# Kernel tuning notes

Measured on AMD Instinct MI355X. Metric: run time of the kernel, lower is better.

Reference implementation:

```python
import jax, jax.numpy as jnp
import numpy as np
from jax import lax

DIM = 128
HEADS = 4
HEAD_DIM = DIM // HEADS          # 32
SR = 2
BN_EPS = 1e-5


def setup_inputs() -> dict:
    key = jax.random.key(0)
    ks = jax.random.split(key, 16)
    B, N, C = 8, 3136, DIM
    H = W = 56
    Nkv = (H // SR) * (W // SR)  # 784
    s = 0.05
    inp = {
        "x": jax.random.normal(ks[0], (B, N, C), jnp.float32),
        "relative_pos": jax.random.normal(ks[1], (HEADS, N, Nkv), jnp.float32),
        "Wq": jax.random.normal(ks[2], (C, C), jnp.float32) * s,
        "bq": jnp.zeros((C,), jnp.float32),
        "Wk": jax.random.normal(ks[3], (C, C), jnp.float32) * s,
        "bk": jnp.zeros((C,), jnp.float32),
        "Wv": jax.random.normal(ks[4], (C, C), jnp.float32) * s,
        "bv": jnp.zeros((C,), jnp.float32),
        "conv_w": jax.random.normal(ks[5], (C, 1, SR, SR), jnp.float32) * s,  # depthwise OIHW
        "conv_b": jnp.zeros((C,), jnp.float32),
        "bn_gamma": jnp.ones((C,), jnp.float32),
        "bn_beta": jnp.zeros((C,), jnp.float32),
        "bn_mean": jax.random.normal(ks[6], (C,), jnp.float32) * 0.1,
        "bn_var": jax.random.uniform(ks[7], (C,), jnp.float32, 0.5, 1.5),
        "Wp": jax.random.normal(ks[8], (C, C), jnp.float32) * s,
        "bp": jnp.zeros((C,), jnp.float32),
        "H": H,
        "W": W,
    }
    return inp


def reference(x, relative_pos, Wq, bq, Wk, bk, Wv, bv, conv_w, conv_b,
              bn_gamma, bn_beta, bn_mean, bn_var, Wp, bp, H, W):
    B, N, C = x.shape
    scale = HEAD_DIM ** -0.5

    # q: (B, heads, N, head_dim)
    q = (x @ Wq + bq).reshape(B, N, HEADS, HEAD_DIM).transpose(0, 2, 1, 3)

    # spatial reduction: depthwise conv stride SR + BatchNorm (eval, running stats)
    x_img = x.transpose(0, 2, 1).reshape(B, C, H, W)
    y = lax.conv_general_dilated(
        x_img, conv_w, window_strides=(SR, SR), padding="VALID",
        feature_group_count=C,
        dimension_numbers=("NCHW", "OIHW", "NCHW")) + conv_b[None, :, None, None]
    inv = bn_gamma * lax.rsqrt(bn_var + BN_EPS)
    y = y * inv[None, :, None, None] + (bn_beta - bn_mean * inv)[None, :, None, None]
    x_ = y.reshape(B, C, -1).transpose(0, 2, 1)  # (B, Nkv, C)
    Nkv = x_.shape[1]

    k = (x_ @ Wk + bk).reshape(B, Nkv, HEADS, HEAD_DIM).transpose(0, 2, 1, 3)
    v = (x_ @ Wv + bv).reshape(B, Nkv, HEADS, HEAD_DIM).transpose(0, 2, 1, 3)

    attn = jnp.einsum("bhnd,bhmd->bhnm", q, k) * scale + relative_pos[None]
    attn = jax.nn.softmax(attn, axis=-1)
    out = jnp.einsum("bhnm,bhmd->bhnd", attn, v)
    out = out.transpose(0, 2, 1, 3).reshape(B, N, C)
    return out @ Wp + bp
```

## Files before the change

kernel.cpp:

```cpp
#include <hip/hip_runtime.h>
#include <hip/hip_bf16.h>

#define BATCH 8
#define NQ 3136
#define CDIM 128
#define NHEAD 4
#define HD 32
#define NKV 784
#define HIMG 56
#define SCALE 0.17677669529663687f

typedef __attribute__((ext_vector_type(8))) short bf8_t;
typedef __attribute__((ext_vector_type(4))) float f4_t;

using bf16 = __hip_bfloat16;
using u16  = unsigned short;

static __device__ __forceinline__ float b2f(bf16 v){ return __bfloat162float(v); }
static __device__ __forceinline__ bf16  f2b(float v){ return __float2bfloat16(v); }
static __device__ __forceinline__ short f2s(float v){
  union { bf16 b; short s; } u; u.b = f2b(v); return u.s;
}
static __device__ __forceinline__ float u16f(u16 x){
  union { u16 u; bf16 b; } c; c.u = x; return b2f(c.b);
}
static __device__ __forceinline__ float ld1(const void* p, size_t i, int f){
  return f ? b2f(((const bf16*)p)[i]) : ((const float*)p)[i];
}
static __device__ __forceinline__ bf8_t ld8(const void* p, size_t i, int f){
  if (f) return *(const bf8_t*)((const bf16*)p + i);
  const float* fp = (const float*)p + i;
  float4 a = *(const float4*)fp;
  float4 b = *(const float4*)(fp + 4);
  bf8_t r;
  r[0]=f2s(a.x); r[1]=f2s(a.y); r[2]=f2s(a.z); r[3]=f2s(a.w);
  r[4]=f2s(b.x); r[5]=f2s(b.y); r[6]=f2s(b.z); r[7]=f2s(b.w);
  return r;
}
static __device__ __forceinline__ int detect_flag(const void* var_raw){
  const u16* h = (const u16*)var_raw;
  int lane = threadIdx.x & 63;
  bool ok = true;
  #pragma unroll
  for (int t = 0; t < 2; t++){
    union { u16 u; bf16 b; } cv; cv.u = h[lane + 64*t];
    float v = b2f(cv.b);
    ok = ok && (v > 0.3f) && (v < 1.7f);
  }
  return (__ballot(ok) == ~0ull) ? 1 : 0;
}

static __device__ __forceinline__ void mfma_row(
    const bf8_t a[4], const bf16* __restrict__ Wt, int m, int g, f4_t acc[8])
{
  #pragma unroll
  for (int ct = 0; ct < 8; ct++){
    f4_t c = {0.f,0.f,0.f,0.f};
    const bf16* bp = Wt + (size_t)(ct*16 + m)*CDIM + 8*g;
    #pragma unroll
    for (int ks = 0; ks < 4; ks++){
      bf8_t b = *(const bf8_t*)(bp + 32*ks);
      c = __builtin_amdgcn_mfma_f32_16x16x32_bf16(a[ks], b, c, 0,0,0);
    }
    acc[ct] = c;
  }
}

__global__ __launch_bounds__(256) void prep_kernel(
    const void* __restrict__ Wq, const void* __restrict__ Wk,
    const void* __restrict__ Wv, const void* __restrict__ Wp,
    const void* __restrict__ var, const void* __restrict__ cw,
    const void* __restrict__ cb, const void* __restrict__ gam,
    const void* __restrict__ bet, const void* __restrict__ mea,
    const void* __restrict__ bq, const void* __restrict__ bk,
    const void* __restrict__ bv, const void* __restrict__ bp,
    bf16* __restrict__ Wqt, bf16* __restrict__ Wkt,
    bf16* __restrict__ Wvt, bf16* __restrict__ Wpt,
    bf16* __restrict__ bqs, bf16* __restrict__ bks,
    bf16* __restrict__ bvs, bf16* __restrict__ bps,
    float* __restrict__ cwf, float* __restrict__ inv, float* __restrict__ shift2)
{
  int f = detect_flag(var);
  int idx = blockIdx.x*256 + threadIdx.x;
  int mat = idx >> 14;
  int e   = idx & 16383;
  int o = e >> 7, i = e & 127;
  const void* src; bf16* dst; float s = 1.f;
  if      (mat == 0){ src = Wq; dst = Wqt; s = SCALE; }
  else if (mat == 1){ src = Wk; dst = Wkt; }
  else if (mat == 2){ src = Wv; dst = Wvt; }
  else              { src = Wp; dst = Wpt; }
  dst[e] = f2b(ld1(src, (size_t)i*128 + o, f) * s);

  if (blockIdx.x == 0){
    int t = threadIdx.x;
    cwf[t]       = ld1(cw, t, f);
    cwf[t + 256] = ld1(cw, t + 256, f);
    if (t < 128){
      bqs[t] = f2b(ld1(bq, t, f) * SCALE);
      bks[t] = f2b(ld1(bk, t, f));
      bvs[t] = f2b(ld1(bv, t, f));
      bps[t] = f2b(ld1(bp, t, f));
      float iv = ld1(gam, t, f) * rsqrtf(ld1(var, t, f) + 1e-5f);
      inv[t] = iv;
      shift2[t] = ld1(bet, t, f) - ld1(mea, t, f) * iv + ld1(cb, t, f) * iv;
    }
  }
}

__global__ __launch_bounds__(256) void fat_kernel(
    const void* __restrict__ x, const void* __restrict__ var,
    const float* __restrict__ cwf, const float* __restrict__ inv,
    const float* __restrict__ shift2, bf16* __restrict__ xr,
    const bf16* __restrict__ Wqt, const bf16* __restrict__ bqs,
    bf16* __restrict__ qbf,
    const void* __restrict__ rel, bf16* __restrict__ relb, int qblk)
{
  int f = detect_flag(var);
  if (blockIdx.x < 3136){
    int idx = blockIdx.x*256 + threadIdx.x;
    int c  = idx & 127;
    int t  = idx >> 7;
    int b  = t / NKV;
    int kv = t - b*NKV;
    int i = kv/28, j = kv - i*28;
    size_t base = (size_t)(b*NQ + 2*i*HIMG + 2*j)*CDIM + c;
    float acc = ld1(x, base, f)                   * cwf[c*4 + 0]
              + ld1(x, base + CDIM, f)            * cwf[c*4 + 1]
              + ld1(x, base + HIMG*CDIM, f)       * cwf[c*4 + 2]
              + ld1(x, base + HIMG*CDIM + CDIM, f)* cwf[c*4 + 3];
    xr[idx] = f2b(acc * inv[c] + shift2[c]);
  } else if ((int)blockIdx.x < 3136 + qblk){
    int wave = threadIdx.x >> 6, lane = threadIdx.x & 63;
    int m = lane & 15, g = lane >> 4;
    int task = (blockIdx.x - 3136)*4 + wave;
    int row0 = task*16;
    bf8_t a[4];
    #pragma unroll
    for (int ks = 0; ks < 4; ks++)
      a[ks] = ld8(x, (size_t)(row0 + m)*CDIM + 8*g + 32*ks, f);
    f4_t acc[8];
    mfma_row(a, Wqt, m, g, acc);
    #pragma unroll
    for (int ct = 0; ct < 8; ct++){
      int col = ct*16 + m;
      float bv = b2f(bqs[col]);
      #pragma unroll
      for (int r = 0; r < 4; r++)
        qbf[(size_t)(row0 + 4*g + r)*CDIM + col] = f2b(acc[ct][r] + bv);
    }
  } else {
    if (f) return;
    int bi = blockIdx.x - 3136 - qblk;
    size_t gid = ((size_t)bi*256 + threadIdx.x)*8;
    const float* fp = (const float*)rel + gid;
    float4 a  = *(const float4*)fp;
    float4 b4 = *(const float4*)(fp + 4);
    union { u16 hh[8]; uint4 u4; } pk;
    pk.hh[0]=(u16)f2s(a.x);  pk.hh[1]=(u16)f2s(a.y);
    pk.hh[2]=(u16)f2s(a.z);  pk.hh[3]=(u16)f2s(a.w);
    pk.hh[4]=(u16)f2s(b4.x); pk.hh[5]=(u16)f2s(b4.y);
    pk.hh[6]=(u16)f2s(b4.z); pk.hh[7]=(u16)f2s(b4.w);
    *(uint4*)(relb + gid) = pk.u4;
  }
}

__global__ __launch_bounds__(256) void kv_kernel(
    const bf16* __restrict__ xr,
    const bf16* __restrict__ Wkt, const bf16* __restrict__ Wvt,
    const bf16* __restrict__ bks, const bf16* __restrict__ bvs,
    bf16* __restrict__ kbf, bf16* __restrict__ vtb)
{
  int wave = threadIdx.x >> 6, lane = threadIdx.x & 63;
  int m = lane & 15, g = lane >> 4;
  bool isK = blockIdx.x < 98;
  int bx = isK ? blockIdx.x : blockIdx.x - 98;
  int row0 = (bx*4 + wave)*16;
  bf8_t a[4];
  #pragma unroll
  for (int ks = 0; ks < 4; ks++)
    a[ks] = *(const bf8_t*)(xr + (size_t)(row0 + m)*CDIM + 8*g + 32*ks);
  f4_t acc[8];
  mfma_row(a, isK ? Wkt : Wvt, m, g, acc);

  if (isK){
    #pragma unroll
    for (int ct = 0; ct < 8; ct++){
      int col = ct*16 + m;
      float bv = b2f(bks[col]);
      #pragma unroll
      for (int r = 0; r < 4; r++)
        kbf[(size_t)(row0 + 4*g + r)*CDIM + col] = f2b(acc[ct][r] + bv);
    }
  } else {
    int b   = row0 / NKV;
    int kv0 = row0 - b*NKV + 4*g;
    #pragma unroll
    for (int ct = 0; ct < 8; ct++){
      int col = ct*16 + m;
      float bv = b2f(bvs[col]);
      int h = col >> 5, d = col & 31;
      union { bf16 hh[4]; uint2 u; } pk;
      #pragma unroll
      for (int r = 0; r < 4; r++) pk.hh[r] = f2b(acc[ct][r] + bv);
      *(uint2*)(vtb + (size_t)((b*NHEAD + h)*HD + d)*NKV + kv0) = pk.u;
    }
  }
}

template<int RM> struct RelT { using T = float4; };
template<> struct RelT<1> { using T = uint2; };

template<int RM>
static __device__ __forceinline__ typename RelT<RM>::T relld(const void* relp, int off){
  if constexpr (RM == 1) return *(const uint2*)((const bf16*)relp + off);
  else                   return *(const float4*)((const float*)relp + off);
}
template<int RM>
static __device__ __forceinline__ float relget(const typename RelT<RM>::T& v, int r){
  if constexpr (RM == 1){
    union { uint2 u; u16 h[4]; } c; c.u = v;
    return u16f(c.h[r]);
  } else {
    return r == 0 ? v.x : (r == 1 ? v.y : (r == 2 ? v.z : v.w));
  }
}

template<int RM>
static __device__ __forceinline__ void attn_run(
    const void* __restrict__ relp, const bf16* __restrict__ kbase,
    const bf16* __restrict__ vb0, const bf16* __restrict__ vb1,
    bf16* __restrict__ pl, int m, int g,
    bf8_t q8, float& m_run, float& l_run, f4_t& O0, f4_t& O1)
{
  using RT = typename RelT<RM>::T;
  RT rl[8], rt;
  #pragma unroll
  for (int t = 0; t < 8; t++) rl[t] = relld<RM>(relp, 16*t + 4*g);

  #pragma unroll 1
  for (int c = 0; c < 6; c++){
    int kv0 = c*128;
    f4_t s[8];
    #pragma unroll
    for (int t = 0; t < 8; t++){
      bf8_t k8 = *(const bf8_t*)(kbase + (size_t)(kv0 + t*16)*CDIM);
      f4_t z = {0.f,0.f,0.f,0.f};
      s[t] = __builtin_amdgcn_mfma_f32_16x16x32_bf16(k8, q8, z, 0,0,0);
    }
    #pragma unroll
    for (int t = 0; t < 8; t++)
      #pragma unroll
      for (int r = 0; r < 4; r++)
        s[t][r] += relget<RM>(rl[t], r);
    if (c < 5){
      #pragma unroll
      for (int t = 0; t < 8; t++)
        rl[t] = relld<RM>(relp, kv0 + 128 + 16*t + 4*g);
    } else {
      rt = relld<RM>(relp, 768 + 4*g);
    }
    float vmax = s[0][0];
    #pragma unroll
    for (int t = 0; t < 8; t++)
      #pragma unroll
      for (int r = 0; r < 4; r++)
        if (t + r > 0) vmax = fmaxf(vmax, s[t][r]);
    vmax = fmaxf(vmax, __shfl_xor(vmax, 16, 64));
    vmax = fmaxf(vmax, __shfl_xor(vmax, 32, 64));
    float mn = fmaxf(m_run, vmax);
    float al = __expf(m_run - mn);
    m_run = mn;
    l_run *= al;
    float alT[4];
    #pragma unroll
    for (int r = 0; r < 4; r++) alT[r] = __shfl(al, 4*g + r, 64);
    #pragma unroll
    for (int r = 0; r < 4; r++){ O0[r] *= alT[r]; O1[r] *= alT[r]; }
    float lsum = 0.f;
    #pragma unroll
    for (int t = 0; t < 8; t++){
      union { u16 h[4]; uint2 u; } pk;
      #pragma unroll
      for (int r = 0; r < 4; r++){
        float p = __expf(s[t][r] - m_run);
        lsum += p;
        pk.h[r] = (u16)f2s(p);
      }
      *(uint2*)(pl + m*136 + 16*t + 4*g) = pk.u;
    }
    l_run += lsum;
    #pragma unroll
    for (int ks = 0; ks < 4; ks++){
      bf8_t a8 = *(const bf8_t*)(pl + m*136 + ks*32 + 8*g);
      bf8_t v0 = *(const bf8_t*)(vb0 + kv0 + ks*32 + 8*g);
      bf8_t v1 = *(const bf8_t*)(vb1 + kv0 + ks*32 + 8*g);
      O0 = __builtin_amdgcn_mfma_f32_16x16x32_bf16(a8, v0, O0, 0,0,0);
      O1 = __builtin_amdgcn_mfma_f32_16x16x32_bf16(a8, v1, O1, 0,0,0);
    }
  }
  {
    bf8_t k8 = *(const bf8_t*)(kbase + (size_t)768*CDIM);
    f4_t z = {0.f,0.f,0.f,0.f};
    f4_t s1 = __builtin_amdgcn_mfma_f32_16x16x32_bf16(k8, q8, z, 0,0,0);
    #pragma unroll
    for (int r = 0; r < 4; r++) s1[r] += relget<RM>(rt, r);
    float vmax = s1[0];
    #pragma unroll
    for (int r = 1; r < 4; r++) vmax = fmaxf(vmax, s1[r]);
    vmax = fmaxf(vmax, __shfl_xor(vmax, 16, 64));
    vmax = fmaxf(vmax, __shfl_xor(vmax, 32, 64));
    float mn = fmaxf(m_run, vmax);
    float al = __expf(m_run - mn);
    m_run = mn;
    l_run *= al;
    float alT[4];
    #pragma unroll
    for (int r = 0; r < 4; r++) alT[r] = __shfl(al, 4*g + r, 64);
    #pragma unroll
    for (int r = 0; r < 4; r++){ O0[r] *= alT[r]; O1[r] *= alT[r]; }
    float lsum = 0.f;
    union { u16 h[4]; uint2 u; } pk;
    #pragma unroll
    for (int r = 0; r < 4; r++){
      float p = __expf(s1[r] - m_run);
      lsum += p;
      pk.h[r] = (u16)f2s(p);
    }
    *(uint2*)(pl + m*136 + 4*g) = pk.u;
    l_run += lsum;
    bf8_t a8, v0, v1;
    if (g >= 2){
      bf8_t z8 = {0,0,0,0,0,0,0,0};
      a8 = z8; v0 = z8; v1 = z8;
    } else {
      a8 = *(const bf8_t*)(pl + m*136 + 8*g);
      v0 = *(const bf8_t*)(vb0 + 768 + 8*g);
      v1 = *(const bf8_t*)(vb1 + 768 + 8*g);
    }
    O0 = __builtin_amdgcn_mfma_f32_16x16x32_bf16(a8, v0, O0, 0,0,0);
    O1 = __builtin_amdgcn_mfma_f32_16x16x32_bf16(a8, v1, O1, 0,0,0);
  }
}

template<int QF>
__global__ __launch_bounds__(256) void attn_kernel(
    const bf16* __restrict__ qbf, const void* __restrict__ x,
    const bf16* __restrict__ Wqt, const bf16* __restrict__ bqs,
    const bf16* __restrict__ kb, const bf16* __restrict__ vtb,
    const void* __restrict__ rel, const bf16* __restrict__ relb,
    const void* __restrict__ var,
    void* __restrict__ dout, bf16* __restrict__ obf)
{
  int f = detect_flag(var);
  int wave = threadIdx.x >> 6, lane = threadIdx.x & 63;
  int m = lane & 15, g = lane >> 4;
  int qt = blockIdx.x, h = blockIdx.y, b = blockIdx.z;
  int qrow0 = qt*64 + wave*16;

  __shared__ bf16 Plds[4][16*136];
  bf16* pl = Plds[wave];

  bf8_t q8;
  if constexpr (QF == 0){
    q8 = *(const bf8_t*)(qbf + (size_t)(b*NQ + qrow0 + m)*CDIM + h*HD + 8*g);
  } else {
    bf8_t xa[4];
    #pragma unroll
    for (int ks = 0; ks < 4; ks++)
      xa[ks] = ld8(x, (size_t)(b*NQ + qrow0 + m)*CDIM + 8*g + 32*ks, f);
    f4_t qc0 = {0.f,0.f,0.f,0.f}, qc1 = {0.f,0.f,0.f,0.f};
    const bf16* wp0 = Wqt + (size_t)(h*HD + m)*CDIM + 8*g;
    const bf16* wp1 = Wqt + (size_t)(h*HD + 16 + m)*CDIM + 8*g;
    #pragma unroll
    for (int ks = 0; ks < 4; ks++){
      bf8_t w0 = *(const bf8_t*)(wp0 + 32*ks);
      bf8_t w1 = *(const bf8_t*)(wp1 + 32*ks);
      qc0 = __builtin_amdgcn_mfma_f32_16x16x32_bf16(xa[ks], w0, qc0, 0,0,0);
      qc1 = __builtin_amdgcn_mfma_f32_16x16x32_bf16(xa[ks], w1, qc1, 0,0,0);
    }
    float bv0 = b2f(bqs[h*HD + m]);
    float bv1 = b2f(bqs[h*HD + 16 + m]);
    #pragma unroll
    for (int r = 0; r < 4; r++){
      pl[(4*g + r)*136 + m]      = f2b(qc0[r] + bv0);
      pl[(4*g + r)*136 + 16 + m] = f2b(qc1[r] + bv1);
    }
    q8 = *(const bf8_t*)(pl + m*136 + 8*g);
  }

  const bf16* kbase = kb  + (size_t)(b*NKV + m)*CDIM + h*HD + 8*g;
  const bf16* vb0   = vtb + (size_t)((b*NHEAD + h)*HD + m)*NKV;
  const bf16* vb1   = vtb + (size_t)((b*NHEAD + h)*HD + 16 + m)*NKV;
  size_t rrow = ((size_t)h*NQ + qrow0 + m)*(size_t)NKV;

  float m_run = -1e30f, l_run = 0.f;
  f4_t O0 = {0.f,0.f,0.f,0.f}, O1 = {0.f,0.f,0.f,0.f};

  if (f){
    attn_run<1>((const void*)((const bf16*)rel + rrow), kbase, vb0, vb1,
                pl, m, g, q8, m_run, l_run, O0, O1);
  } else if (relb != nullptr){
    attn_run<1>((const void*)(relb + rrow), kbase, vb0, vb1,
                pl, m, g, q8, m_run, l_run, O0, O1);
  } else {
    attn_run<0>((const void*)((const float*)rel + rrow), kbase, vb0, vb1,
                pl, m, g, q8, m_run, l_run, O0, O1);
  }

  l_run += __shfl_xor(l_run, 16, 64);
  l_run += __shfl_xor(l_run, 32, 64);
  float lT[4];
  #pragma unroll
  for (int r = 0; r < 4; r++) lT[r] = __shfl(l_run, 4*g + r, 64);

  bf16* ob = f ? (bf16*)dout : obf;
  size_t orow = (size_t)(b*NQ + qrow0 + 4*g);
  #pragma unroll
  for (int r = 0; r < 4; r++){
    float iv = 1.0f / lT[r];
    ob[(orow + r)*CDIM + h*HD + m]      = f2b(O0[r] * iv);
    ob[(orow + r)*CDIM + h*HD + 16 + m] = f2b(O1[r] * iv);
  }
}

__global__ __launch_bounds__(256) void proj_kernel(
    const bf16* A0, const bf16* A1, const bf16* __restrict__ Wt,
    const bf16* __restrict__ bias, void* outp, const void* __restrict__ var)
{
  int f = detect_flag(var);
  const bf16* A = f ? A0 : A1;
  int wave = threadIdx.x >> 6, lane = threadIdx.x & 63;
  int m = lane & 15, g = lane >> 4;
  int row0 = (blockIdx.x*4 + wave)*16;
  bf8_t a[4];
  #pragma unroll
  for (int ks = 0; ks < 4; ks++)
    a[ks] = *(const bf8_t*)(A + (size_t)(row0 + m)*CDIM + 8*g + 32*ks);
  f4_t acc[8];
  mfma_row(a, Wt, m, g, acc);
  #pragma unroll
  for (int ct = 0; ct < 8; ct++){
    int col = ct*16 + m;
    float bv = b2f(bias[col]);
    #pragma unroll
    for (int r = 0; r < 4; r++){
      size_t oi = (size_t)(row0 + 4*g + r)*CDIM + col;
      float v = acc[ct][r] + bv;
      if (f) ((bf16*)outp)[oi]  = f2b(v);
      else   ((float*)outp)[oi] = v;
    }
  }
}

extern "C" void kernel_launch(void* const* d_in, const int* in_sizes, int n_in,
                              void* d_out, int out_size, void* d_ws, size_t ws_size,
                              hipStream_t stream)
{
  const void* x   = d_in[0];
  const void* rel = d_in[1];
  const void* Wq  = d_in[2];
  const void* bq  = d_in[3];
  const void* Wk  = d_in[4];
  const void* bk  = d_in[5];
  const void* Wv  = d_in[6];
  const void* bv  = d_in[7];
  const void* cw  = d_in[8];
  const void* cb  = d_in[9];
  const void* gam = d_in[10];
  const void* bet = d_in[11];
  const void* mea = d_in[12];
  const void* var = d_in[13];
  const void* Wp  = d_in[14];
  const void* bp  = d_in[15];

  char* w = (char*)d_ws;
  auto alloc = [&](size_t bytes){
    char* p = w; w += (bytes + 255) & ~(size_t)255; return p;
  };
  bf16* Wqt = (bf16*)alloc(128*128*sizeof(bf16));
  bf16* Wkt = (bf16*)alloc(128*128*sizeof(bf16));
  bf16* Wvt = (bf16*)alloc(128*128*sizeof(bf16));
  bf16* Wpt = (bf16*)alloc(128*128*sizeof(bf16));
  bf16* bqs = (bf16*)alloc(128*sizeof(bf16));
  bf16* bks = (bf16*)alloc(128*sizeof(bf16));
  bf16* bvs = (bf16*)alloc(128*sizeof(bf16));
  bf16* bps = (bf16*)alloc(128*sizeof(bf16));
  float* cwf    = (float*)alloc(512*sizeof(float));
  float* inv    = (float*)alloc(128*sizeof(float));
  float* shift2 = (float*)alloc(128*sizeof(float));
  bf16* xr  = (bf16*)alloc((size_t)BATCH*NKV*CDIM*sizeof(bf16));
  bf16* kbf = (bf16*)alloc((size_t)BATCH*NKV*CDIM*sizeof(bf16));
  bf16* vtb = (bf16*)alloc((size_t)BATCH*NKV*CDIM*sizeof(bf16));
  bf16* obf = (bf16*)alloc((size_t)BATCH*NQ*CDIM*sizeof(bf16));

  size_t relb_bytes = (size_t)NHEAD*NQ*NKV*sizeof(bf16);
  bf16* relb = nullptr;
  if (((char*)d_ws + ws_size) - w >= (ptrdiff_t)(relb_bytes + 256))
    relb = (bf16*)alloc(relb_bytes);

  size_t qbf_bytes = (size_t)BATCH*NQ*CDIM*sizeof(bf16);
  bool use_q = (((char*)d_ws + ws_size) - w) >= (ptrdiff_t)(qbf_bytes + 256);
  bf16* qbf = use_q ? (bf16*)alloc(qbf_bytes) : nullptr;

  int qblk = use_q ? 392 : 0;
  int rblk = relb  ? 4802 : 0;

  prep_kernel<<<256, 256, 0, stream>>>(Wq, Wk, Wv, Wp, var, cw, cb, gam, bet, mea,
                                       bq, bk, bv, bp,
                                       Wqt, Wkt, Wvt, Wpt, bqs, bks, bvs, bps,
                                       cwf, inv, shift2);
  fat_kernel<<<3136 + qblk + rblk, 256, 0, stream>>>(
      x, var, cwf, inv, shift2, xr, Wqt, bqs, qbf, rel, relb, qblk);
  kv_kernel<<<196, 256, 0, stream>>>(xr, Wkt, Wvt, bks, bvs, kbf, vtb);
  dim3 ag(49, NHEAD, BATCH);
  if (use_q)
    attn_kernel<0><<<ag, 256, 0, stream>>>(
        qbf, x, Wqt, bqs, kbf, vtb, rel, relb, var, d_out, obf);
  else
    attn_kernel<1><<<ag, 256, 0, stream>>>(
        qbf, x, Wqt, bqs, kbf, vtb, rel, relb, var, d_out, obf);
  proj_kernel<<<392, 256, 0, stream>>>((const bf16*)d_out, obf, Wpt, bps, d_out, var);
}
```

Measured before the change: 230.5 us.

## Split attention KV chunks to 64, transpose PV MFMA, vectorize conv reduction

The attention inner loop now processes 64-key chunks instead of 128, with double-buffered relative-position prefetch, and a launch-bounds hint asks for more waves per SIMD. Swapping the MFMA operand order for P·V puts the output row-wise per lane. That removes the cross-lane shuffles for the rescale factor and the final normalisation, and lets the output be written as packed 4-element stores. The depthwise conv/BN stage processes 4 channels per thread with float4 loads and a transposed weight layout, cutting its block count by four. The catch is more online-softmax rescale steps per row, and register pressure under the tighter launch bound may cause spills.

```diff
diff --git a/kernel.cpp b/kernel.cpp
--- a/kernel.cpp
+++ b/kernel.cpp
@@ -26,6 +26,13 @@
 }
 static __device__ __forceinline__ float ld1(const void* p, size_t i, int f){
   return f ? b2f(((const bf16*)p)[i]) : ((const float*)p)[i];
+}
+static __device__ __forceinline__ float4 ld4f(const void* p, size_t i, int f){
+  if (f){
+    ushort4 u = *(const ushort4*)((const bf16*)p + i);
+    return make_float4(u16f(u.x), u16f(u.y), u16f(u.z), u16f(u.w));
+  }
+  return *(const float4*)((const float*)p + i);
 }
 static __device__ __forceinline__ bf8_t ld8(const void* p, size_t i, int f){
   if (f) return *(const bf8_t*)((const bf16*)p + i);
@@ -94,8 +101,8 @@
 
   if (blockIdx.x == 0){
     int t = threadIdx.x;
-    cwf[t]       = ld1(cw, t, f);
-    cwf[t + 256] = ld1(cw, t + 256, f);
+    { int e2 = t;       cwf[(e2&3)*128 + (e2>>2)] = ld1(cw, e2, f); }
+    { int e2 = t + 256; cwf[(e2&3)*128 + (e2>>2)] = ld1(cw, e2, f); }
     if (t < 128){
       bqs[t] = f2b(ld1(bq, t, f) * SCALE);
       bks[t] = f2b(ld1(bk, t, f));
@@ -117,23 +124,35 @@
     const void* __restrict__ rel, bf16* __restrict__ relb, int qblk)
 {
   int f = detect_flag(var);
-  if (blockIdx.x < 3136){
+  if (blockIdx.x < 784){
     int idx = blockIdx.x*256 + threadIdx.x;
-    int c  = idx & 127;
-    int t  = idx >> 7;
+    int c0 = (idx & 31)*4;
+    int t  = idx >> 5;
     int b  = t / NKV;
     int kv = t - b*NKV;
     int i = kv/28, j = kv - i*28;
-    size_t base = (size_t)(b*NQ + 2*i*HIMG + 2*j)*CDIM + c;
-    float acc = ld1(x, base, f)                   * cwf[c*4 + 0]
-              + ld1(x, base + CDIM, f)            * cwf[c*4 + 1]
-              + ld1(x, base + HIMG*CDIM, f)       * cwf[c*4 + 2]
-              + ld1(x, base + HIMG*CDIM + CDIM, f)* cwf[c*4 + 3];
-    xr[idx] = f2b(acc * inv[c] + shift2[c]);
-  } else if ((int)blockIdx.x < 3136 + qblk){
+    size_t base = (size_t)(b*NQ + 2*i*HIMG + 2*j)*CDIM + c0;
+    float4 t0 = ld4f(x, base, f);
+    float4 t1 = ld4f(x, base + CDIM, f);
+    float4 t2 = ld4f(x, base + HIMG*CDIM, f);
+    float4 t3 = ld4f(x, base + HIMG*CDIM + CDIM, f);
+    float4 w0 = *(const float4*)(cwf + c0);
+    float4 w1 = *(const float4*)(cwf + 128 + c0);
+    float4 w2 = *(const float4*)(cwf + 256 + c0);
+    float4 w3 = *(const float4*)(cwf + 384 + c0);
+    float4 iv4 = *(const float4*)(inv + c0);
+    float4 sh4 = *(const float4*)(shift2 + c0);
+    union { u16 h[4]; uint2 u; } pk;
+    float a;
+    a = t0.x*w0.x + t1.x*w1.x + t2.x*w2.x + t3.x*w3.x; pk.h[0] = (u16)f2s(a*iv4.x + sh4.x);
+    a = t0.y*w0.y + t1.y*w1.y + t2.y*w2.y + t3.y*w3.y; pk.h[1] = (u16)f2s(a*iv4.y + sh4.y);
+    a = t0.z*w0.z + t1.z*w1.z + t2.z*w2.z + t3.z*w3.z; pk.h[2] = (u16)f2s(a*iv4.z + sh4.z);
+    a = t0.w*w0.w + t1.w*w1.w + t2.w*w2.w + t3.w*w3.w; pk.h[3] = (u16)f2s(a*iv4.w + sh4.w);
+    *(uint2*)(xr + (size_t)t*CDIM + c0) = pk.u;
+  } else if ((int)blockIdx.x < 784 + qblk){
     int wave = threadIdx.x >> 6, lane = threadIdx.x & 63;
     int m = lane & 15, g = lane >> 4;
-    int task = (blockIdx.x - 3136)*4 + wave;
+    int task = (blockIdx.x - 784)*4 + wave;
     int row0 = task*16;
     bf8_t a[4];
     #pragma unroll
@@ -151,7 +170,7 @@
     }
   } else {
     if (f) return;
-    int bi = blockIdx.x - 3136 - qblk;
+    int bi = blockIdx.x - 784 - qblk;
     size_t gid = ((size_t)bi*256 + threadIdx.x)*8;
     const float* fp = (const float*)rel + gid;
     float4 a  = *(const float4*)fp;
@@ -208,21 +227,83 @@
   }
 }
 
-template<int RM> struct RelT { using T = float4; };
-template<> struct RelT<1> { using T = uint2; };
+template<int RM> struct RelV { using T = float4; };
+template<> struct RelV<1> { using T = uint2; };
 
 template<int RM>
-static __device__ __forceinline__ typename RelT<RM>::T relld(const void* relp, int off){
+static __device__ __forceinline__ typename RelV<RM>::T relld(const void* relp, int off){
   if constexpr (RM == 1) return *(const uint2*)((const bf16*)relp + off);
   else                   return *(const float4*)((const float*)relp + off);
 }
 template<int RM>
-static __device__ __forceinline__ float relget(const typename RelT<RM>::T& v, int r){
+static __device__ __forceinline__ float relget(const typename RelV<RM>::T& v, int r){
   if constexpr (RM == 1){
     union { uint2 u; u16 h[4]; } c; c.u = v;
     return u16f(c.h[r]);
   } else {
     return r == 0 ? v.x : (r == 1 ? v.y : (r == 2 ? v.z : v.w));
+  }
+}
+template<int RM>
+static __device__ __forceinline__ void ldrel4(
+    typename RelV<RM>::T rl[4], const void* relp, int off){
+  #pragma unroll
+  for (int t = 0; t < 4; t++) rl[t] = relld<RM>(relp, off + 16*t);
+}
+
+template<int RM>
+static __device__ __forceinline__ void chunk64(
+    int kv0, const typename RelV<RM>::T rl[4],
+    const bf16* __restrict__ kbase, const bf16* __restrict__ vb0,
+    const bf16* __restrict__ vb1, bf16* __restrict__ pl, int m, int g,
+    bf8_t q8, float& m_run, float& l_run, f4_t& O0, f4_t& O1)
+{
+  f4_t s[4];
+  #pragma unroll
+  for (int t = 0; t < 4; t++){
+    bf8_t k8 = *(const bf8_t*)(kbase + (size_t)(kv0 + t*16)*CDIM);
+    f4_t z = {0.f,0.f,0.f,0.f};
+    s[t] = __builtin_amdgcn_mfma_f32_16x16x32_bf16(k8, q8, z, 0,0,0);
+  }
+  #pragma unroll
+  for (int t = 0; t < 4; t++)
+    #pragma unroll
+    for (int r = 0; r < 4; r++)
+      s[t][r] += relget<RM>(rl[t], r);
+  float vmax = s[0][0];
+  #pragma unroll
+  for (int t = 0; t < 4; t++)
+    #pragma unroll
+    for (int r = 0; r < 4; r++)
+      if (t + r > 0) vmax = fmaxf(vmax, s[t][r]);
+  vmax = fmaxf(vmax, __shfl_xor(vmax, 16, 64));
+  vmax = fmaxf(vmax, __shfl_xor(vmax, 32, 64));
+  float mn = fmaxf(m_run, vmax);
+  float al = __expf(m_run - mn);
+  m_run = mn;
+  l_run *= al;
+  #pragma unroll
+  for (int r = 0; r < 4; r++){ O0[r] *= al; O1[r] *= al; }
+  float lsum = 0.f;
+  #pragma unroll
+  for (int t = 0; t < 4; t++){
+    union { u16 h[4]; uint2 u; } pk;
+    #pragma unroll
+    for (int r = 0; r < 4; r++){
+      float p = __expf(s[t][r] - m_run);
+      lsum += p;
+      pk.h[r] = (u16)f2s(p);
+    }
+    *(uint2*)(pl + m*136 + t*16 + 4*g) = pk.u;
+  }
+  l_run += lsum;
+  #pragma unroll
+  for (int ks = 0; ks < 2; ks++){
+    bf8_t a8 = *(const bf8_t*)(pl + m*136 + ks*32 + 8*g);
+    bf8_t v0 = *(const bf8_t*)(vb0 + kv0 + ks*32 + 8*g);
+    bf8_t v1 = *(const bf8_t*)(vb1 + kv0 + ks*32 + 8*g);
+    O0 = __builtin_amdgcn_mfma_f32_16x16x32_bf16(v0, a8, O0, 0,0,0);
+    O1 = __builtin_amdgcn_mfma_f32_16x16x32_bf16(v1, a8, O1, 0,0,0);
   }
 }
 
@@ -233,94 +314,35 @@
     bf16* __restrict__ pl, int m, int g,
     bf8_t q8, float& m_run, float& l_run, f4_t& O0, f4_t& O1)
 {
-  using RT = typename RelT<RM>::T;
-  RT rl[8], rt;
-  #pragma unroll
-  for (int t = 0; t < 8; t++) rl[t] = relld<RM>(relp, 16*t + 4*g);
-
+  using RT = typename RelV<RM>::T;
+  RT rlA[4], rlB[4], rtv;
+  ldrel4<RM>(rlA, relp, 4*g);
   #pragma unroll 1
-  for (int c = 0; c < 6; c++){
-    int kv0 = c*128;
-    f4_t s[8];
-    #pragma unroll
-    for (int t = 0; t < 8; t++){
-      bf8_t k8 = *(const bf8_t*)(kbase + (size_t)(kv0 + t*16)*CDIM);
-      f4_t z = {0.f,0.f,0.f,0.f};
-      s[t] = __builtin_amdgcn_mfma_f32_16x16x32_bf16(k8, q8, z, 0,0,0);
-    }
-    #pragma unroll
-    for (int t = 0; t < 8; t++)
-      #pragma unroll
-      for (int r = 0; r < 4; r++)
-        s[t][r] += relget<RM>(rl[t], r);
-    if (c < 5){
-      #pragma unroll
-      for (int t = 0; t < 8; t++)
-        rl[t] = relld<RM>(relp, kv0 + 128 + 16*t + 4*g);
-    } else {
-      rt = relld<RM>(relp, 768 + 4*g);
-    }
-    float vmax = s[0][0];
-    #pragma unroll
-    for (int t = 0; t < 8; t++)
-      #pragma unroll
-      for (int r = 0; r < 4; r++)
-        if (t + r > 0) vmax = fmaxf(vmax, s[t][r]);
+  for (int c2 = 0; c2 < 6; c2++){
+    int kv0 = c2*128;
+    ldrel4<RM>(rlB, relp, kv0 + 64 + 4*g);
+    chunk64<RM>(kv0, rlA, kbase, vb0, vb1, pl, m, g, q8, m_run, l_run, O0, O1);
+    if (c2 < 5) ldrel4<RM>(rlA, relp, kv0 + 128 + 4*g);
+    else        rtv = relld<RM>(relp, 768 + 4*g);
+    chunk64<RM>(kv0 + 64, rlB, kbase, vb0, vb1, pl, m, g, q8, m_run, l_run, O0, O1);
+  }
+  {
+    bf8_t k8 = *(const bf8_t*)(kbase + (size_t)768*CDIM);
+    f4_t z = {0.f,0.f,0.f,0.f};
+    f4_t s1 = __builtin_amdgcn_mfma_f32_16x16x32_bf16(k8, q8, z, 0,0,0);
+    #pragma unroll
+    for (int r = 0; r < 4; r++) s1[r] += relget<RM>(rtv, r);
+    float vmax = fmaxf(fmaxf(s1[0], s1[1]), fmaxf(s1[2], s1[3]));
     vmax = fmaxf(vmax, __shfl_xor(vmax, 16, 64));
     vmax = fmaxf(vmax, __shfl_xor(vmax, 32, 64));
     float mn = fmaxf(m_run, vmax);
     float al = __expf(m_run - mn);
     m_run = mn;
     l_run *= al;
-    float alT[4];
-    #pragma unroll
-    for (int r = 0; r < 4; r++) alT[r] = __shfl(al, 4*g + r, 64);
-    #pragma unroll
-    for (int r = 0; r < 4; r++){ O0[r] *= alT[r]; O1[r] *= alT[r]; }
+    #pragma unroll
+    for (int r = 0; r < 4; r++){ O0[r] *= al; O1[r] *= al; }
+    union { u16 h[4]; uint2 u; } pk;
     float lsum = 0.f;
-    #pragma unroll
-    for (int t = 0; t < 8; t++){
-      union { u16 h[4]; uint2 u; } pk;
-      #pragma unroll
-      for (int r = 0; r < 4; r++){
-        float p = __expf(s[t][r] - m_run);
-        lsum += p;
-        pk.h[r] = (u16)f2s(p);
-      }
-      *(uint2*)(pl + m*136 + 16*t + 4*g) = pk.u;
-    }
-    l_run += lsum;
-    #pragma unroll
-    for (int ks = 0; ks < 4; ks++){
-      bf8_t a8 = *(const bf8_t*)(pl + m*136 + ks*32 + 8*g);
-      bf8_t v0 = *(const bf8_t*)(vb0 + kv0 + ks*32 + 8*g);
-      bf8_t v1 = *(const bf8_t*)(vb1 + kv0 + ks*32 + 8*g);
-      O0 = __builtin_amdgcn_mfma_f32_16x16x32_bf16(a8, v0, O0, 0,0,0);
-      O1 = __builtin_amdgcn_mfma_f32_16x16x32_bf16(a8, v1, O1, 0,0,0);
-    }
-  }
-  {
-    bf8_t k8 = *(const bf8_t*)(kbase + (size_t)768*CDIM);
-    f4_t z = {0.f,0.f,0.f,0.f};
-    f4_t s1 = __builtin_amdgcn_mfma_f32_16x16x32_bf16(k8, q8, z, 0,0,0);
-    #pragma unroll
-    for (int r = 0; r < 4; r++) s1[r] += relget<RM>(rt, r);
-    float vmax = s1[0];
-    #pragma unroll
-    for (int r = 1; r < 4; r++) vmax = fmaxf(vmax, s1[r]);
-    vmax = fmaxf(vmax, __shfl_xor(vmax, 16, 64));
-    vmax = fmaxf(vmax, __shfl_xor(vmax, 32, 64));
-    float mn = fmaxf(m_run, vmax);
-    float al = __expf(m_run - mn);
-    m_run = mn;
-    l_run *= al;
-    float alT[4];
-    #pragma unroll
-    for (int r = 0; r < 4; r++) alT[r] = __shfl(al, 4*g + r, 64);
-    #pragma unroll
-    for (int r = 0; r < 4; r++){ O0[r] *= alT[r]; O1[r] *= alT[r]; }
-    float lsum = 0.f;
-    union { u16 h[4]; uint2 u; } pk;
     #pragma unroll
     for (int r = 0; r < 4; r++){
       float p = __expf(s1[r] - m_run);
@@ -338,13 +360,13 @@
       v0 = *(const bf8_t*)(vb0 + 768 + 8*g);
       v1 = *(const bf8_t*)(vb1 + 768 + 8*g);
     }
-    O0 = __builtin_amdgcn_mfma_f32_16x16x32_bf16(a8, v0, O0, 0,0,0);
-    O1 = __builtin_amdgcn_mfma_f32_16x16x32_bf16(a8, v1, O1, 0,0,0);
-  }
-}
-
-template<int QF>
-__global__ __launch_bounds__(256) void attn_kernel(
+    O0 = __builtin_amdgcn_mfma_f32_16x16x32_bf16(v0, a8, O0, 0,0,0);
+    O1 = __builtin_amdgcn_mfma_f32_16x16x32_bf16(v1, a8, O1, 0,0,0);
+  }
+}
+
+template<int QF, int FB>
+static __device__ __forceinline__ void attn_device(
     const bf16* __restrict__ qbf, const void* __restrict__ x,
     const bf16* __restrict__ Wqt, const bf16* __restrict__ bqs,
     const bf16* __restrict__ kb, const bf16* __restrict__ vtb,
@@ -397,31 +419,54 @@
   float m_run = -1e30f, l_run = 0.f;
   f4_t O0 = {0.f,0.f,0.f,0.f}, O1 = {0.f,0.f,0.f,0.f};
 
-  if (f){
-    attn_run<1>((const void*)((const bf16*)rel + rrow), kbase, vb0, vb1,
-                pl, m, g, q8, m_run, l_run, O0, O1);
-  } else if (relb != nullptr){
-    attn_run<1>((const void*)(relb + rrow), kbase, vb0, vb1,
-                pl, m, g, q8, m_run, l_run, O0, O1);
+  if constexpr (FB == 0){
+    const void* rsrc = f ? (const void*)((const bf16*)rel + rrow)
+                         : (const void*)(relb + rrow);
+    attn_run<1>(rsrc, kbase, vb0, vb1, pl, m, g, q8, m_run, l_run, O0, O1);
   } else {
-    attn_run<0>((const void*)((const float*)rel + rrow), kbase, vb0, vb1,
-                pl, m, g, q8, m_run, l_run, O0, O1);
+    if (f) attn_run<1>((const void*)((const bf16*)rel + rrow), kbase, vb0, vb1,
+                       pl, m, g, q8, m_run, l_run, O0, O1);
+    else   attn_run<0>((const void*)((const float*)rel + rrow), kbase, vb0, vb1,
+                       pl, m, g, q8, m_run, l_run, O0, O1);
   }
 
   l_run += __shfl_xor(l_run, 16, 64);
   l_run += __shfl_xor(l_run, 32, 64);
-  float lT[4];
-  #pragma unroll
-  for (int r = 0; r < 4; r++) lT[r] = __shfl(l_run, 4*g + r, 64);
-
-  bf16* ob = f ? (bf16*)dout : obf;
-  size_t orow = (size_t)(b*NQ + qrow0 + 4*g);
+  float iv = 1.0f / l_run;
+
+  bf16* ob = (f ? (bf16*)dout : obf)
+           + (size_t)(b*NQ + qrow0 + m)*CDIM + h*HD;
+  union { u16 h4[4]; uint2 u; } o0, o1;
   #pragma unroll
   for (int r = 0; r < 4; r++){
-    float iv = 1.0f / lT[r];
-    ob[(orow + r)*CDIM + h*HD + m]      = f2b(O0[r] * iv);
-    ob[(orow + r)*CDIM + h*HD + 16 + m] = f2b(O1[r] * iv);
-  }
+    o0.h4[r] = (u16)f2s(O0[r] * iv);
+    o1.h4[r] = (u16)f2s(O1[r] * iv);
+  }
+  *(uint2*)(ob + 4*g)      = o0.u;
+  *(uint2*)(ob + 16 + 4*g) = o1.u;
+}
+
+template<int QF>
+__global__ __launch_bounds__(256, 6) void attn_kernel(
+    const bf16* __restrict__ qbf, const void* __restrict__ x,
+    const bf16* __restrict__ Wqt, const bf16* __restrict__ bqs,
+    const bf16* __restrict__ kb, const bf16* __restrict__ vtb,
+    const void* __restrict__ rel, const bf16* __restrict__ relb,
+    const void* __restrict__ var,
+    void* __restrict__ dout, bf16* __restrict__ obf)
+{
+  attn_device<QF,0>(qbf, x, Wqt, bqs, kb, vtb, rel, relb, var, dout, obf);
+}
+
+__global__ __launch_bounds__(256) void attn_kernel_fb(
+    const bf16* __restrict__ qbf, const void* __restrict__ x,
+    const bf16* __restrict__ Wqt, const bf16* __restrict__ bqs,
+    const bf16* __restrict__ kb, const bf16* __restrict__ vtb,
+    const void* __restrict__ rel, const bf16* __restrict__ relb,
+    const void* __restrict__ var,
+    void* __restrict__ dout, bf16* __restrict__ obf)
+{
+  attn_device<1,1>(qbf, x, Wqt, bqs, kb, vtb, rel, relb, var, dout, obf);
 }
 
 __global__ __launch_bounds__(256) void proj_kernel(
@@ -500,7 +545,8 @@
     relb = (bf16*)alloc(relb_bytes);
 
   size_t qbf_bytes = (size_t)BATCH*NQ*CDIM*sizeof(bf16);
-  bool use_q = (((char*)d_ws + ws_size) - w) >= (ptrdiff_t)(qbf_bytes + 256);
+  bool use_q = relb &&
+      ((((char*)d_ws + ws_size) - w) >= (ptrdiff_t)(qbf_bytes + 256));
   bf16* qbf = use_q ? (bf16*)alloc(qbf_bytes) : nullptr;
 
   int qblk = use_q ? 392 : 0;
@@ -510,15 +556,20 @@
                                        bq, bk, bv, bp,
                                        Wqt, Wkt, Wvt, Wpt, bqs, bks, bvs, bps,
                                        cwf, inv, shift2);
-  fat_kernel<<<3136 + qblk + rblk, 256, 0, stream>>>(
+  fat_kernel<<<784 + qblk + rblk, 256, 0, stream>>>(
       x, var, cwf, inv, shift2, xr, Wqt, bqs, qbf, rel, relb, qblk);
   kv_kernel<<<196, 256, 0, stream>>>(xr, Wkt, Wvt, bks, bvs, kbf, vtb);
   dim3 ag(49, NHEAD, BATCH);
-  if (use_q)
-    attn_kernel<0><<<ag, 256, 0, stream>>>(
+  if (relb){
+    if (use_q)
+      attn_kernel<0><<<ag, 256, 0, stream>>>(
+          qbf, x, Wqt, bqs, kbf, vtb, rel, relb, var, d_out, obf);
+    else
+      attn_kernel<1><<<ag, 256, 0, stream>>>(
+          qbf, x, Wqt, bqs, kbf, vtb, rel, relb, var, d_out, obf);
+  } else {
+    attn_kernel_fb<<<ag, 256, 0, stream>>>(
         qbf, x, Wqt, bqs, kbf, vtb, rel, relb, var, d_out, obf);
-  else
-    attn_kernel<1><<<ag, 256, 0, stream>>>(
-        qbf, x, Wqt, bqs, kbf, vtb, rel, relb, var, d_out, obf);
+  }
   proj_kernel<<<392, 256, 0, stream>>>((const bf16*)d_out, obf, Wpt, bps, d_out, var);
 }
```

Result: slower. 236.3 us (+2.5%).
